# Performance work log

Hardware: AMD Instinct MI355X
Metric: run time of the kernel (lower is better)

Reference implementation:

```python
import jax, jax.numpy as jnp
import numpy as np

B, CIN, COUT, H, W_SP = 16, 128, 128, 56, 56
E, KH, KW = 4, 3, 3

def setup_inputs() -> dict:
    key = jax.random.key(0)
    k1, k2, k3 = jax.random.split(key, 3)
    x = jax.random.normal(k1, (B, CIN, H, W_SP), dtype=jnp.float32)
    routing_weights = jax.random.uniform(k2, (B, E), dtype=jnp.float32)
    # expert conv kernels, OIHW, stacked over experts: [E, COUT, CIN, KH, KW]
    W = jax.random.normal(k3, (E, COUT, CIN, KH, KW), dtype=jnp.float32) * 0.05
    return {"x": x, "routing_weights": routing_weights, "W": W}

def reference(x, routing_weights, W):
    # Each expert: full Conv2d(stride=1, padding=1, dilation=1, groups=1, no bias)
    def one_expert(w):  # w: [COUT, CIN, KH, KW]
        return jax.lax.conv_general_dilated(
            x, w,
            window_strides=(1, 1),
            padding=((1, 1), (1, 1)),
            dimension_numbers=("NCHW", "OIHW", "NCHW"),
        )
    expert_outs = jax.vmap(one_expert)(W)  # [E, B, COUT, H, W]
    # per-sample scalar mix: sum_e routing[b, e] * expert_outs[e, b]
    out = jnp.einsum("ebchw,be->bchw", expert_outs, routing_weights)
    return out
```

## Files before the change

### kernel.cpp

```cpp
#include <hip/hip_runtime.h>


typedef float  f32x16 __attribute__((ext_vector_type(16)));
typedef short  s16x8  __attribute__((ext_vector_type(8)));
typedef unsigned short u16;

#define CIN   128
#define COUT  128
#define HH    56
#define WW    56
#define SP    (HH*WW)
#define EW    147456
#define BW_   147456
#define XSTR  72
#define XB    (4*66*XSTR)
#define AB    8192

static __device__ __forceinline__ u16 f2bf(float f) {
    unsigned u = __builtin_bit_cast(unsigned, f);
    return (u16)((u + 0x7FFFu + ((u >> 16) & 1u)) >> 16);
}

static __device__ __forceinline__ void gload16(const void* g, void* l) {
    __builtin_amdgcn_global_load_lds(
        (const __attribute__((address_space(1))) void*)g,
        (__attribute__((address_space(3))) void*)l, 16, 0, 0);
}

__global__ __launch_bounds__(256) void mix_kernel(const float* __restrict__ W,
                                                  const float* __restrict__ r,
                                                  u16* __restrict__ Wmix) {
    int o = blockIdx.x * 256 + threadIdx.x;
    int ci_l = o & 31;
    int o2   = o >> 5;
    int co   = o2 & 127;
    int o3   = o2 >> 7;
    int tap  = o3 % 9;
    int cc   = o3 / 9;
    size_t src = ((size_t)co * CIN + cc*32 + ci_l) * 9 + tap;
    float w0 = W[src], w1 = W[src + EW], w2 = W[src + 2*EW], w3 = W[src + 3*EW];
    #pragma unroll
    for (int b = 0; b < 16; ++b) {
        float acc = r[b*4+0]*w0 + r[b*4+1]*w1 + r[b*4+2]*w2 + r[b*4+3]*w3;
        Wmix[(size_t)b * BW_ + o] = f2bf(acc);
    }
}

__global__ __launch_bounds__(512, 4) void conv_mfma(const float* __restrict__ x,
                                                    const u16* __restrict__ Wmix,
                                                    float* __restrict__ out) {
    __shared__ __align__(16) char ldsb[XB + 4*AB];

    const int bid = blockIdx.x;
    const int bs  = (bid & 7) * 56 + (bid >> 3);
    const int b   = bs / 28;
    const int ph  = bs % 28;
    const int t    = threadIdx.x;
    const int lane = t & 63;
    const int wid  = t >> 6;
    const int wm   = (wid >> 2) & 1;
    const int wn   = (wid >> 1) & 1;
    const int wp   = wid & 1;
    const int l31  = lane & 31;
    const int khalf= lane >> 5;

    const u16*   WmixB = Wmix + (size_t)b * BW_;
    const float* xbB   = x + (size_t)b * CIN * SP;

    const int ssl = (t & 3) ^ ((t >> 3) & 3);

    f32x16 acc[2];
    acc[0] = (f32x16)0.f;
    acc[1] = (f32x16)0.f;

    auto stageA = [&](int it) {
        char* ldst = ldsb + XB + (it & 3) * AB + wid * 1024;
        const u16* ga = WmixB + it * 4096 + (t >> 2) * 32 + ssl * 8;
        gload16(ga, ldst);
    };

    auto stageX = [&](int cc) {
        #pragma unroll
        for (int i = 0; i < 2; ++i) {
            int slot = i * 512 + t;
            int c    = 1 + (slot & 63);
            int row  = (slot >> 6) & 3;
            int g    = slot >> 8;
            int rr   = 2*ph - 1 + row;
            int w    = c - 1;
            bool ok  = ((unsigned)rr < 56u) && (w < 56);
            const float* p = xbB + (size_t)(cc*32 + g*8) * SP + rr*56 + w;
            s16x8 v;
            #pragma unroll
            for (int j = 0; j < 8; ++j) {
                float f = ok ? p[(size_t)j * SP] : 0.f;
                v[j] = (short)f2bf(f);
            }
            *(s16x8*)(ldsb + (row*66 + c)*XSTR + g*16) = v;
        }
    };

    auto compute = [&](int it, int kh, int kw) {
        const char* Ab = ldsb + XB + (it & 3) * AB;
        #pragma unroll
        for (int ksub = 0; ksub < 2; ++ksub) {
            const int s = ksub * 2 + khalf;
            s16x8 af[2], bv;
            #pragma unroll
            for (int mf = 0; mf < 2; ++mf)
                af[mf] = *(const s16x8*)(Ab + (wm*64 + mf*32 + l31)*64
                                            + ((s ^ ((l31 >> 1) & 3)) * 16));
            const int c = wp*32 + l31 + kw;
            bv = *(const s16x8*)(ldsb + ((wn + kh)*66 + c)*XSTR + s*16);
            #pragma unroll
            for (int mf = 0; mf < 2; ++mf)
                acc[mf] = __builtin_amdgcn_mfma_f32_32x32x16_bf16(
                    af[mf], bv, acc[mf], 0, 0, 0);
        }
    };

    if (t < 32) {
        int row = t >> 3, col = ((t >> 2) & 1) ? 65 : 0, sl = t & 3;
        *(s16x8*)(ldsb + (row*66 + col)*XSTR + sl*16) = (s16x8)0;
    }
    stageA(0);
    stageA(1);
    stageX(0);
    asm volatile("s_waitcnt lgkmcnt(0)" ::: "memory");
    __builtin_amdgcn_sched_barrier(0);
    __builtin_amdgcn_s_barrier();
    __builtin_amdgcn_sched_barrier(0);

    #pragma unroll
    for (int cc = 0; cc < 4; ++cc) {
        if (cc) {
            __builtin_amdgcn_sched_barrier(0);
            __builtin_amdgcn_s_barrier();
            __builtin_amdgcn_sched_barrier(0);
            stageX(cc);
            asm volatile("s_waitcnt lgkmcnt(0)" ::: "memory");
            __builtin_amdgcn_sched_barrier(0);
            __builtin_amdgcn_s_barrier();
            __builtin_amdgcn_sched_barrier(0);
        }
        #pragma unroll
        for (int tap = 0; tap < 9; ++tap) {
            const int it = cc * 9 + tap;
            if (it + 2 < 36) {
                stageA(it + 2);
                asm volatile("s_waitcnt vmcnt(2)" ::: "memory");
            } else if (it + 1 < 36) {
                asm volatile("s_waitcnt vmcnt(1)" ::: "memory");
            } else {
                asm volatile("s_waitcnt vmcnt(0)" ::: "memory");
            }
            __builtin_amdgcn_s_barrier();
            __builtin_amdgcn_sched_barrier(0);
            __builtin_amdgcn_s_setprio(1);
            compute(it, tap / 3, tap % 3);
            __builtin_amdgcn_s_setprio(0);
        }
    }

    const int w = wp * 32 + l31;
    if (w < 56) {
        const int hrow = 2 * ph + wn;
        #pragma unroll
        for (int mf = 0; mf < 2; ++mf) {
            #pragma unroll
            for (int rg = 0; rg < 16; ++rg) {
                int co = wm*64 + mf*32 + (rg & 3) + 8*(rg >> 2) + 4*khalf;
                out[(((size_t)b*COUT + co)*HH + hrow)*WW + w] = acc[mf][rg];
            }
        }
    }
}

extern "C" void kernel_launch(void* const* d_in, const int* in_sizes, int n_in,
                              void* d_out, int out_size, void* d_ws, size_t ws_size,
                              hipStream_t stream) {
    const float* x = (const float*)d_in[0];
    const float* r = (const float*)d_in[1];
    const float* W = (const float*)d_in[2];
    float* outp = (float*)d_out;
    u16* Wmix = (u16*)d_ws;

    mix_kernel<<<576, 256, 0, stream>>>(W, r, Wmix);
    conv_mfma <<<448, 512, 0, stream>>>(x, Wmix, outp);
}
```

Baseline: 34.47 us.

## Split conv tiles by width halves to double blocks and raise occupancy

```diff
diff --git a/kernel.cpp b/kernel.cpp
--- a/kernel.cpp
+++ b/kernel.cpp
@@ -13,7 +13,7 @@
 #define EW    147456
 #define BW_   147456
 #define XSTR  72
-#define XB    (4*66*XSTR)
+#define XB2   (4*34*XSTR)
 #define AB    8192
 
 static __device__ __forceinline__ u16 f2bf(float f) {
@@ -46,21 +46,23 @@
     }
 }
 
-__global__ __launch_bounds__(512, 4) void conv_mfma(const float* __restrict__ x,
+__global__ __launch_bounds__(512, 6) void conv_mfma(const float* __restrict__ x,
                                                     const u16* __restrict__ Wmix,
                                                     float* __restrict__ out) {
-    __shared__ __align__(16) char ldsb[XB + 4*AB];
+    __shared__ __align__(16) char ldsb[XB2 + 4*AB];
 
     const int bid = blockIdx.x;
-    const int bs  = (bid & 7) * 56 + (bid >> 3);
-    const int b   = bs / 28;
-    const int ph  = bs % 28;
+    const int bs  = (bid & 7) * 112 + (bid >> 3);
+    const int b   = bs / 56;
+    const int rem = bs % 56;
+    const int ph  = rem >> 1;
+    const int pxh = rem & 1;
+    const int w0  = pxh * 32;
     const int t    = threadIdx.x;
     const int lane = t & 63;
     const int wid  = t >> 6;
-    const int wm   = (wid >> 2) & 1;
-    const int wn   = (wid >> 1) & 1;
-    const int wp   = wid & 1;
+    const int wc   = wid & 3;
+    const int wn   = wid >> 2;
     const int l31  = lane & 31;
     const int khalf= lane >> 5;
 
@@ -69,26 +71,23 @@
 
     const int ssl = (t & 3) ^ ((t >> 3) & 3);
 
-    f32x16 acc[2];
-    acc[0] = (f32x16)0.f;
-    acc[1] = (f32x16)0.f;
+    f32x16 acc = (f32x16)0.f;
 
     auto stageA = [&](int it) {
-        char* ldst = ldsb + XB + (it & 3) * AB + wid * 1024;
+        char* ldst = ldsb + XB2 + (it & 3) * AB + wid * 1024;
         const u16* ga = WmixB + it * 4096 + (t >> 2) * 32 + ssl * 8;
         gload16(ga, ldst);
     };
 
     auto stageX = [&](int cc) {
-        #pragma unroll
-        for (int i = 0; i < 2; ++i) {
-            int slot = i * 512 + t;
-            int c    = 1 + (slot & 63);
-            int row  = (slot >> 6) & 3;
-            int g    = slot >> 8;
+        for (int s = t; s < 544; s += 512) {
+            int c    = s % 34;
+            int rest = s / 34;
+            int row  = rest & 3;
+            int g    = rest >> 2;
             int rr   = 2*ph - 1 + row;
-            int w    = c - 1;
-            bool ok  = ((unsigned)rr < 56u) && (w < 56);
+            int w    = w0 + c - 1;
+            bool ok  = ((unsigned)rr < 56u) && ((unsigned)w < 56u);
             const float* p = xbB + (size_t)(cc*32 + g*8) * SP + rr*56 + w;
             s16x8 v;
             #pragma unroll
@@ -96,33 +95,27 @@
                 float f = ok ? p[(size_t)j * SP] : 0.f;
                 v[j] = (short)f2bf(f);
             }
-            *(s16x8*)(ldsb + (row*66 + c)*XSTR + g*16) = v;
+            *(s16x8*)(ldsb + (row*34 + c)*XSTR + g*16) = v;
         }
     };
 
-    auto compute = [&](int it, int kh, int kw) {
-        const char* Ab = ldsb + XB + (it & 3) * AB;
+    auto compute = [&](int n, int kh, int kw) {
+        const char* Ab = ldsb + XB2 + (n & 3) * AB;
+        s16x8 af[2], bv[2];
         #pragma unroll
         for (int ksub = 0; ksub < 2; ++ksub) {
             const int s = ksub * 2 + khalf;
-            s16x8 af[2], bv;
-            #pragma unroll
-            for (int mf = 0; mf < 2; ++mf)
-                af[mf] = *(const s16x8*)(Ab + (wm*64 + mf*32 + l31)*64
-                                            + ((s ^ ((l31 >> 1) & 3)) * 16));
-            const int c = wp*32 + l31 + kw;
-            bv = *(const s16x8*)(ldsb + ((wn + kh)*66 + c)*XSTR + s*16);
-            #pragma unroll
-            for (int mf = 0; mf < 2; ++mf)
-                acc[mf] = __builtin_amdgcn_mfma_f32_32x32x16_bf16(
-                    af[mf], bv, acc[mf], 0, 0, 0);
+            af[ksub] = *(const s16x8*)(Ab + (wc*32 + l31)*64
+                                          + ((s ^ ((l31 >> 1) & 3)) * 16));
+            const int c = l31 + kw;
+            bv[ksub] = *(const s16x8*)(ldsb + ((wn + kh)*34 + c)*XSTR + s*16);
         }
+        #pragma unroll
+        for (int ksub = 0; ksub < 2; ++ksub)
+            acc = __builtin_amdgcn_mfma_f32_32x32x16_bf16(af[ksub], bv[ksub],
+                                                          acc, 0, 0, 0);
     };
 
-    if (t < 32) {
-        int row = t >> 3, col = ((t >> 2) & 1) ? 65 : 0, sl = t & 3;
-        *(s16x8*)(ldsb + (row*66 + col)*XSTR + sl*16) = (s16x8)0;
-    }
     stageA(0);
     stageA(1);
     stageX(0);
@@ -145,11 +138,11 @@
         }
         #pragma unroll
         for (int tap = 0; tap < 9; ++tap) {
-            const int it = cc * 9 + tap;
-            if (it + 2 < 36) {
-                stageA(it + 2);
+            const int n = cc * 9 + tap;
+            if (n + 2 < 36) {
+                stageA(n + 2);
                 asm volatile("s_waitcnt vmcnt(2)" ::: "memory");
-            } else if (it + 1 < 36) {
+            } else if (n + 1 < 36) {
                 asm volatile("s_waitcnt vmcnt(1)" ::: "memory");
             } else {
                 asm volatile("s_waitcnt vmcnt(0)" ::: "memory");
@@ -157,21 +150,18 @@
             __builtin_amdgcn_s_barrier();
             __builtin_amdgcn_sched_barrier(0);
             __builtin_amdgcn_s_setprio(1);
-            compute(it, tap / 3, tap % 3);
+            compute(n, tap / 3, tap % 3);
             __builtin_amdgcn_s_setprio(0);
         }
     }
 
-    const int w = wp * 32 + l31;
+    const int w = w0 + l31;
     if (w < 56) {
         const int hrow = 2 * ph + wn;
         #pragma unroll
-        for (int mf = 0; mf < 2; ++mf) {
-            #pragma unroll
-            for (int rg = 0; rg < 16; ++rg) {
-                int co = wm*64 + mf*32 + (rg & 3) + 8*(rg >> 2) + 4*khalf;
-                out[(((size_t)b*COUT + co)*HH + hrow)*WW + w] = acc[mf][rg];
-            }
+        for (int rg = 0; rg < 16; ++rg) {
+            int co = wc*32 + (rg & 3) + 8*(rg >> 2) + 4*khalf;
+            out[(((size_t)b*COUT + co)*HH + hrow)*WW + w] = acc[rg];
         }
     }
 }
@@ -186,5 +176,5 @@
     u16* Wmix = (u16*)d_ws;
 
     mix_kernel<<<576, 256, 0, stream>>>(W, r, Wmix);
-    conv_mfma <<<448, 512, 0, stream>>>(x, Wmix, outp);
+    conv_mfma <<<896, 512, 0, stream>>>(x, Wmix, outp);
 }
```

After: 41.58 us. 1.21x slower.

## Stage weights three taps at a time with double-buffered windows

Applied to the files above, without the earlier changes.

```diff
diff --git a/kernel.cpp b/kernel.cpp
--- a/kernel.cpp
+++ b/kernel.cpp
@@ -14,7 +14,7 @@
 #define BW_   147456
 #define XSTR  72
 #define XB    (4*66*XSTR)
-#define AB    8192
+#define WINB  24576
 
 static __device__ __forceinline__ u16 f2bf(float f) {
     unsigned u = __builtin_bit_cast(unsigned, f);
@@ -49,7 +49,7 @@
 __global__ __launch_bounds__(512, 4) void conv_mfma(const float* __restrict__ x,
                                                     const u16* __restrict__ Wmix,
                                                     float* __restrict__ out) {
-    __shared__ __align__(16) char ldsb[XB + 4*AB];
+    __shared__ __align__(16) char ldsb[XB + 2*WINB];
 
     const int bid = blockIdx.x;
     const int bs  = (bid & 7) * 56 + (bid >> 3);
@@ -73,10 +73,12 @@
     acc[0] = (f32x16)0.f;
     acc[1] = (f32x16)0.f;
 
-    auto stageA = [&](int it) {
-        char* ldst = ldsb + XB + (it & 3) * AB + wid * 1024;
-        const u16* ga = WmixB + it * 4096 + (t >> 2) * 32 + ssl * 8;
-        gload16(ga, ldst);
+    auto stageA3 = [&](int w) {
+        char* buf = ldsb + XB + (w & 1) * WINB + wid * 1024;
+        const u16* ga = WmixB + (size_t)(3*w) * 4096 + (t >> 2) * 32 + ssl * 8;
+        gload16(ga,        buf);
+        gload16(ga + 4096, buf + 8192);
+        gload16(ga + 8192, buf + 16384);
     };
 
     auto stageX = [&](int cc) {
@@ -100,22 +102,25 @@
         }
     };
 
-    auto compute = [&](int it, int kh, int kw) {
-        const char* Ab = ldsb + XB + (it & 3) * AB;
+    auto compute3 = [&](int w) {
+        const char* Ab = ldsb + XB + (w & 1) * WINB;
         #pragma unroll
-        for (int ksub = 0; ksub < 2; ++ksub) {
-            const int s = ksub * 2 + khalf;
-            s16x8 af[2], bv;
+        for (int j = 0; j < 3; ++j) {
+            const int tap = (w % 3) * 3 + j;
+            const int kh  = tap / 3;
+            const int kw  = tap % 3;
             #pragma unroll
-            for (int mf = 0; mf < 2; ++mf)
-                af[mf] = *(const s16x8*)(Ab + (wm*64 + mf*32 + l31)*64
-                                            + ((s ^ ((l31 >> 1) & 3)) * 16));
-            const int c = wp*32 + l31 + kw;
-            bv = *(const s16x8*)(ldsb + ((wn + kh)*66 + c)*XSTR + s*16);
-            #pragma unroll
-            for (int mf = 0; mf < 2; ++mf)
-                acc[mf] = __builtin_amdgcn_mfma_f32_32x32x16_bf16(
-                    af[mf], bv, acc[mf], 0, 0, 0);
+            for (int ksub = 0; ksub < 2; ++ksub) {
+                const int s = ksub * 2 + khalf;
+                s16x8 af0 = *(const s16x8*)(Ab + j*8192 + (wm*64 + l31)*64
+                                               + ((s ^ ((l31 >> 1) & 3)) * 16));
+                s16x8 af1 = *(const s16x8*)(Ab + j*8192 + (wm*64 + 32 + l31)*64
+                                               + ((s ^ ((l31 >> 1) & 3)) * 16));
+                const int c = wp*32 + l31 + kw;
+                s16x8 bv  = *(const s16x8*)(ldsb + ((wn + kh)*66 + c)*XSTR + s*16);
+                acc[0] = __builtin_amdgcn_mfma_f32_32x32x16_bf16(af0, bv, acc[0], 0, 0, 0);
+                acc[1] = __builtin_amdgcn_mfma_f32_32x32x16_bf16(af1, bv, acc[1], 0, 0, 0);
+            }
         }
     };
 
@@ -123,43 +128,30 @@
         int row = t >> 3, col = ((t >> 2) & 1) ? 65 : 0, sl = t & 3;
         *(s16x8*)(ldsb + (row*66 + col)*XSTR + sl*16) = (s16x8)0;
     }
-    stageA(0);
-    stageA(1);
+    stageA3(0);
     stageX(0);
-    asm volatile("s_waitcnt lgkmcnt(0)" ::: "memory");
+    asm volatile("s_waitcnt vmcnt(0) lgkmcnt(0)" ::: "memory");
     __builtin_amdgcn_sched_barrier(0);
     __builtin_amdgcn_s_barrier();
     __builtin_amdgcn_sched_barrier(0);
 
     #pragma unroll
-    for (int cc = 0; cc < 4; ++cc) {
-        if (cc) {
-            __builtin_amdgcn_sched_barrier(0);
-            __builtin_amdgcn_s_barrier();
-            __builtin_amdgcn_sched_barrier(0);
-            stageX(cc);
+    for (int w = 0; w < 12; ++w) {
+        if (w && (w % 3) == 0) {
+            stageX(w / 3);
             asm volatile("s_waitcnt lgkmcnt(0)" ::: "memory");
             __builtin_amdgcn_sched_barrier(0);
             __builtin_amdgcn_s_barrier();
             __builtin_amdgcn_sched_barrier(0);
         }
-        #pragma unroll
-        for (int tap = 0; tap < 9; ++tap) {
-            const int it = cc * 9 + tap;
-            if (it + 2 < 36) {
-                stageA(it + 2);
-                asm volatile("s_waitcnt vmcnt(2)" ::: "memory");
-            } else if (it + 1 < 36) {
-                asm volatile("s_waitcnt vmcnt(1)" ::: "memory");
-            } else {
-                asm volatile("s_waitcnt vmcnt(0)" ::: "memory");
-            }
-            __builtin_amdgcn_s_barrier();
-            __builtin_amdgcn_sched_barrier(0);
-            __builtin_amdgcn_s_setprio(1);
-            compute(it, tap / 3, tap % 3);
-            __builtin_amdgcn_s_setprio(0);
-        }
+        if (w + 1 < 12) stageA3(w + 1);
+        __builtin_amdgcn_s_setprio(1);
+        compute3(w);
+        __builtin_amdgcn_s_setprio(0);
+        asm volatile("s_waitcnt vmcnt(0)" ::: "memory");
+        __builtin_amdgcn_sched_barrier(0);
+        __builtin_amdgcn_s_barrier();
+        __builtin_amdgcn_sched_barrier(0);
     }
 
     const int w = wp * 32 + l31;
```

After: 34.80 us. No clear change (+1.0%).
